# Kernel tuning notes

Measured on AMD Instinct MI355X. Metric: run time of the kernel, lower is better.

## Reference

```python
import jax, jax.numpy as jnp
import numpy as np

ALPHA = 0.25
GAMMA = 2.0

B, A, C, M = 8, 120000, 80, 24


def setup_inputs() -> dict:
    key = jax.random.key(0)
    k1, k2, k3, k4, k5, k6, k7, k8 = jax.random.split(key, 8)
    # classification probabilities in (0,1)
    classifications = jax.random.uniform(k1, (B, A, C), dtype=jnp.float32)
    regressions = jax.random.normal(k2, (B, A, 4), dtype=jnp.float32)
    # anchors: valid x1y1x2y2 boxes on an ~800px canvas
    ctr = jax.random.uniform(k3, (A, 2), minval=0.0, maxval=800.0)
    wh = jax.random.uniform(k4, (A, 2), minval=16.0, maxval=256.0)
    anchors = jnp.concatenate([ctr - 0.5 * wh, ctr + 0.5 * wh], axis=1)[None].astype(jnp.float32)
    # annotations: [B, M, 5] = (x1, y1, x2, y2, label) with -1 label padding
    xy1 = jax.random.uniform(k5, (B, M, 2), minval=0.0, maxval=600.0)
    gwh = jax.random.uniform(k6, (B, M, 2), minval=10.0, maxval=180.0)
    labels = jax.random.randint(k7, (B, M), 0, C).astype(jnp.float32)
    pad = jax.random.uniform(k8, (B, M)) < 0.25
    pad = pad.at[:, 0].set(False)  # guarantee >=1 valid GT per image
    labels = jnp.where(pad, -1.0, labels)
    annots = jnp.concatenate([xy1, xy1 + gwh, labels[..., None]], axis=2).astype(jnp.float32)
    return {"classifications": classifications, "regressions": regressions,
            "anchors": anchors, "annots": annots}


def _box_iou(a, g):
    # a: [A,4], g: [M,4] -> [A,M]
    g_area = (g[:, 2] - g[:, 0]) * (g[:, 3] - g[:, 1])
    a_area = (a[:, 2] - a[:, 0]) * (a[:, 3] - a[:, 1])
    iw = jnp.clip(jnp.minimum(a[:, None, 2], g[None, :, 2]) - jnp.maximum(a[:, None, 0], g[None, :, 0]), 0.0)
    ih = jnp.clip(jnp.minimum(a[:, None, 3], g[None, :, 3]) - jnp.maximum(a[:, None, 1], g[None, :, 1]), 0.0)
    inter = iw * ih
    union = jnp.clip(a_area[:, None] + g_area[None, :] - inter, 1e-6)
    return inter / union


def _per_image(cls_p, reg, annot, anchor, a_w, a_h, a_cx, a_cy):
    cls_p = jnp.clip(cls_p, 1e-4, 1.0 - 1e-4)
    valid = annot[:, 4] >= 0.0  # [M]
    iou = jnp.where(valid[None, :], _box_iou(anchor, annot[:, :4]), -1.0)  # [A,M]
    iou_max = iou.max(axis=1)
    iou_arg = iou.argmax(axis=1)
    pos = iou_max >= 0.5
    neg = iou_max < 0.4
    ignore = ~(pos | neg)

    assigned = annot[iou_arg]  # [A,5] gather of best GT per anchor
    labels = assigned[:, 4].astype(jnp.int32)
    onehot = jax.nn.one_hot(labels, cls_p.shape[1], dtype=cls_p.dtype)
    # -1 = ignored, 1 = positive class, 0 elsewhere
    targets = jnp.where(ignore[:, None], -1.0, onehot * pos[:, None].astype(cls_p.dtype))

    is_pos_t = targets == 1.0
    alpha_f = jnp.where(is_pos_t, ALPHA, 1.0 - ALPHA)
    focal_w = alpha_f * jnp.where(is_pos_t, 1.0 - cls_p, cls_p) ** GAMMA
    ce = -(targets * jnp.log(cls_p) + (1.0 - targets) * jnp.log(1.0 - cls_p))
    cls_loss = jnp.where(targets != -1.0, focal_w * ce, 0.0).sum()
    n_pos = pos.sum()
    cls_loss = cls_loss / jnp.maximum(n_pos.astype(cls_p.dtype), 1.0)

    gt_w = jnp.clip(assigned[:, 2] - assigned[:, 0], 1.0)
    gt_h = jnp.clip(assigned[:, 3] - assigned[:, 1], 1.0)
    gt_cx = assigned[:, 0] + 0.5 * (assigned[:, 2] - assigned[:, 0])
    gt_cy = assigned[:, 1] + 0.5 * (assigned[:, 3] - assigned[:, 1])
    t = jnp.stack([(gt_cx - a_cx) / a_w, (gt_cy - a_cy) / a_h,
                   jnp.log(gt_w / a_w), jnp.log(gt_h / a_h)], axis=1)
    t = t / jnp.array([0.1, 0.1, 0.2, 0.2], dtype=cls_p.dtype)
    diff = jnp.abs(t - reg)
    sl1 = jnp.where(diff <= 1.0 / 9.0, 0.5 * 9.0 * diff * diff, diff - 0.5 / 9.0)
    reg_sum = (sl1 * pos[:, None].astype(cls_p.dtype)).sum()
    denom = jnp.maximum(n_pos * 4, 1).astype(cls_p.dtype)  # mean over [P,4]
    reg_loss = jnp.where(n_pos > 0, reg_sum / denom, 0.0)
    return cls_loss, reg_loss


def reference(classifications, regressions, anchors, annots):
    anchor = anchors[0]
    a_w = anchor[:, 2] - anchor[:, 0]
    a_h = anchor[:, 3] - anchor[:, 1]
    a_cx = anchor[:, 0] + 0.5 * a_w
    a_cy = anchor[:, 1] + 0.5 * a_h
    cls_l, reg_l = jax.vmap(_per_image, in_axes=(0, 0, 0, None, None, None, None, None))(
        classifications, regressions, annots, anchor, a_w, a_h, a_cx, a_cy)
    return cls_l.mean(keepdims=True), reg_l.mean(keepdims=True)
```

## Files before the change

### kernel.cpp

```cpp
#include <hip/hip_runtime.h>
#include <cstdint>

#define B_ 8
#define A_ 120000
#define C_ 80
#define M_ 24
#define APB 250
#define NVB (APB * C_ / 4)


__global__ __launch_bounds__(256) void focal_main(
    const float* __restrict__ cls,
    const float* __restrict__ regs,
    const float* __restrict__ anchors,
    const float* __restrict__ annots,
    float* __restrict__ ws)
{
    const int b   = blockIdx.y;
    const int a0  = blockIdx.x * APB;
    const int tid = threadIdx.x;

    __shared__ float s_annot[M_ * 5];
    __shared__ float s_mask[APB];
    __shared__ float s_redc[4], s_redr[4], s_redp[4];

    if (tid < M_ * 5) s_annot[tid] = annots[b * M_ * 5 + tid];
    __syncthreads();

    float cls_part = 0.0f, reg_part = 0.0f, pos_part = 0.0f;
    const float PLO = 1e-4f, PHI = 1.0f - 1e-4f;

    if (tid < APB) {
        const int a = a0 + tid;
        const float4 ab = *reinterpret_cast<const float4*>(anchors + (size_t)a * 4);
        const float ax1 = ab.x, ay1 = ab.y, ax2 = ab.z, ay2 = ab.w;
        const float aw  = ax2 - ax1, ah = ay2 - ay1;
        const float acx = ax1 + 0.5f * aw, acy = ay1 + 0.5f * ah;
        const float a_area = aw * ah;

        float best = -1e30f;
        int bestm = 0;
        #pragma unroll
        for (int m = 0; m < M_; ++m) {
            const float gx1 = s_annot[m * 5 + 0], gy1 = s_annot[m * 5 + 1];
            const float gx2 = s_annot[m * 5 + 2], gy2 = s_annot[m * 5 + 3];
            const float lab = s_annot[m * 5 + 4];
            const float g_area = (gx2 - gx1) * (gy2 - gy1);
            float iw = fminf(ax2, gx2) - fmaxf(ax1, gx1); iw = fmaxf(iw, 0.0f);
            float ih = fminf(ay2, gy2) - fmaxf(ay1, gy1); ih = fmaxf(ih, 0.0f);
            const float inter = iw * ih;
            const float uni = fmaxf(a_area + g_area - inter, 1e-6f);
            float iou = inter * __builtin_amdgcn_rcpf(uni);
            iou = (lab >= 0.0f) ? iou : -1.0f;
            if (iou > best) { best = iou; bestm = m; }
        }

        const bool pos    = best >= 0.5f;
        const bool ignore = (best >= 0.4f) && !pos;
        const int  lab    = (int)s_annot[bestm * 5 + 4];
        s_mask[tid] = ignore ? 0.0f : 1.0f;

        if (pos) {
            pos_part = 1.0f;
            const float4 rv = *reinterpret_cast<const float4*>(regs + ((size_t)b * A_ + a) * 4);
            const float gx1 = s_annot[bestm * 5 + 0], gy1 = s_annot[bestm * 5 + 1];
            const float gx2 = s_annot[bestm * 5 + 2], gy2 = s_annot[bestm * 5 + 3];
            const float gw  = fmaxf(gx2 - gx1, 1.0f);
            const float gh  = fmaxf(gy2 - gy1, 1.0f);
            const float gcx = gx1 + 0.5f * (gx2 - gx1);
            const float gcy = gy1 + 0.5f * (gy2 - gy1);
            const float inv_aw = __builtin_amdgcn_rcpf(aw);
            const float inv_ah = __builtin_amdgcn_rcpf(ah);
            const float t0 = (gcx - acx) * inv_aw * 10.0f;
            const float t1 = (gcy - acy) * inv_ah * 10.0f;
            const float t2 = __logf(gw * inv_aw) * 5.0f;
            const float t3 = __logf(gh * inv_ah) * 5.0f;
            const float d0 = fabsf(t0 - rv.x), d1 = fabsf(t1 - rv.y);
            const float d2 = fabsf(t2 - rv.z), d3 = fabsf(t3 - rv.w);
            const float th = 1.0f / 9.0f, sub = 0.5f / 9.0f;
            float s;
            s  = (d0 <= th) ? 4.5f * d0 * d0 : d0 - sub;
            s += (d1 <= th) ? 4.5f * d1 * d1 : d1 - sub;
            s += (d2 <= th) ? 4.5f * d2 * d2 : d2 - sub;
            s += (d3 <= th) ? 4.5f * d3 * d3 : d3 - sub;
            reg_part = s;

            float p = cls[((size_t)b * A_ + a) * C_ + lab];
            p = fminf(fmaxf(p, PLO), PHI);
            const float q = 1.0f - p;
            const float pos_term = 0.25f * q * q * (-__logf(p));
            const float neg_term = 0.75f * p * p * (-__logf(q));
            cls_part = pos_term - neg_term;
        }
    }
    __syncthreads();

    const float4* cp4 = reinterpret_cast<const float4*>(cls + ((size_t)b * A_ + a0) * C_);
    const float NEG_SCALE = -0.75f * 0.69314718056f;
    #pragma unroll 4
    for (int i = tid; i < NVB; i += 256) {
        const float4 v = cp4[i];
        const int   al = i / 20;
        const float m  = s_mask[al];
        float c = 0.0f, p, q;
        p = fminf(fmaxf(v.x, PLO), PHI); q = 1.0f - p; c = fmaf(p * p, __log2f(q), c);
        p = fminf(fmaxf(v.y, PLO), PHI); q = 1.0f - p; c = fmaf(p * p, __log2f(q), c);
        p = fminf(fmaxf(v.z, PLO), PHI); q = 1.0f - p; c = fmaf(p * p, __log2f(q), c);
        p = fminf(fmaxf(v.w, PLO), PHI); q = 1.0f - p; c = fmaf(p * p, __log2f(q), c);
        cls_part = fmaf(m * c, NEG_SCALE, cls_part);
    }

    for (int off = 32; off > 0; off >>= 1) {
        cls_part += __shfl_down(cls_part, off, 64);
        reg_part += __shfl_down(reg_part, off, 64);
        pos_part += __shfl_down(pos_part, off, 64);
    }
    const int wid = tid >> 6;
    if ((tid & 63) == 0) { s_redc[wid] = cls_part; s_redr[wid] = reg_part; s_redp[wid] = pos_part; }
    __syncthreads();
    if (tid == 0) {
        atomicAdd(&ws[b],      s_redc[0] + s_redc[1] + s_redc[2] + s_redc[3]);
        atomicAdd(&ws[8 + b],  s_redr[0] + s_redr[1] + s_redr[2] + s_redr[3]);
        atomicAdd(&ws[16 + b], s_redp[0] + s_redp[1] + s_redp[2] + s_redp[3]);
    }
}

__global__ void focal_final(const float* __restrict__ ws, float* __restrict__ out)
{
    if (threadIdx.x == 0) {
        float cm = 0.0f, rm = 0.0f;
        for (int b = 0; b < B_; ++b) {
            const float np = ws[16 + b];
            cm += ws[b] / fmaxf(np, 1.0f);
            rm += (np > 0.0f) ? ws[8 + b] / (np * 4.0f) : 0.0f;
        }
        out[0] = cm * (1.0f / B_);
        out[1] = rm * (1.0f / B_);
    }
}

extern "C" void kernel_launch(void* const* d_in, const int* in_sizes, int n_in,
                              void* d_out, int out_size, void* d_ws, size_t ws_size,
                              hipStream_t stream)
{
    const float* cls     = (const float*)d_in[0];
    const float* regs    = (const float*)d_in[1];
    const float* anchors = (const float*)d_in[2];
    const float* annots  = (const float*)d_in[3];
    float* ws  = (float*)d_ws;
    float* out = (float*)d_out;

    hipMemsetAsync(d_ws, 0, 24 * sizeof(float), stream);

    dim3 grid(A_ / APB, B_);
    focal_main<<<grid, 256, 0, stream>>>(cls, regs, anchors, annots, ws);
    focal_final<<<1, 64, 0, stream>>>(ws, out);
}
```

Measured before the change: 449.6 us.

## Split anchor assignment and class-loss streaming into separate kernels via global mask

The fused kernel becomes two kernels. The first assigns an IoU match to each anchor and writes the ignore mask to workspace memory. The second streams the 307 MB classification tensor with full 256-thread occupancy, fixed 5-wide unrolling and no idle threads, where the old kernel had only 250 of 256 threads active in the assignment phase. The change adds a kernel launch and a global mask round trip, and it drops the lower clamp on p, relying on inputs being positive.

```diff
diff --git a/kernel.cpp b/kernel.cpp
--- a/kernel.cpp
+++ b/kernel.cpp
@@ -5,11 +5,10 @@
 #define A_ 120000
 #define C_ 80
 #define M_ 24
-#define APB 250
-#define NVB (APB * C_ / 4)
 
+#define WS_MASK_OFF 32
 
-__global__ __launch_bounds__(256) void focal_main(
+__global__ __launch_bounds__(256, 4) void assign_k(
     const float* __restrict__ cls,
     const float* __restrict__ regs,
     const float* __restrict__ anchors,
@@ -17,11 +16,10 @@
     float* __restrict__ ws)
 {
     const int b   = blockIdx.y;
-    const int a0  = blockIdx.x * APB;
     const int tid = threadIdx.x;
+    const int a   = blockIdx.x * 256 + tid;
 
     __shared__ float s_annot[M_ * 5];
-    __shared__ float s_mask[APB];
     __shared__ float s_redc[4], s_redr[4], s_redp[4];
 
     if (tid < M_ * 5) s_annot[tid] = annots[b * M_ * 5 + tid];
@@ -30,8 +28,7 @@
     float cls_part = 0.0f, reg_part = 0.0f, pos_part = 0.0f;
     const float PLO = 1e-4f, PHI = 1.0f - 1e-4f;
 
-    if (tid < APB) {
-        const int a = a0 + tid;
+    if (a < A_) {
         const float4 ab = *reinterpret_cast<const float4*>(anchors + (size_t)a * 4);
         const float ax1 = ab.x, ay1 = ab.y, ax2 = ab.z, ay2 = ab.w;
         const float aw  = ax2 - ax1, ah = ay2 - ay1;
@@ -58,7 +55,7 @@
         const bool pos    = best >= 0.5f;
         const bool ignore = (best >= 0.4f) && !pos;
         const int  lab    = (int)s_annot[bestm * 5 + 4];
-        s_mask[tid] = ignore ? 0.0f : 1.0f;
+        ws[WS_MASK_OFF + (size_t)b * A_ + a] = ignore ? 0.0f : 1.0f;
 
         if (pos) {
             pos_part = 1.0f;
@@ -88,26 +85,8 @@
             float p = cls[((size_t)b * A_ + a) * C_ + lab];
             p = fminf(fmaxf(p, PLO), PHI);
             const float q = 1.0f - p;
-            const float pos_term = 0.25f * q * q * (-__logf(p));
-            const float neg_term = 0.75f * p * p * (-__logf(q));
-            cls_part = pos_term - neg_term;
+            cls_part = 0.25f * q * q * (-__logf(p)) - 0.75f * p * p * (-__logf(q));
         }
-    }
-    __syncthreads();
-
-    const float4* cp4 = reinterpret_cast<const float4*>(cls + ((size_t)b * A_ + a0) * C_);
-    const float NEG_SCALE = -0.75f * 0.69314718056f;
-    #pragma unroll 4
-    for (int i = tid; i < NVB; i += 256) {
-        const float4 v = cp4[i];
-        const int   al = i / 20;
-        const float m  = s_mask[al];
-        float c = 0.0f, p, q;
-        p = fminf(fmaxf(v.x, PLO), PHI); q = 1.0f - p; c = fmaf(p * p, __log2f(q), c);
-        p = fminf(fmaxf(v.y, PLO), PHI); q = 1.0f - p; c = fmaf(p * p, __log2f(q), c);
-        p = fminf(fmaxf(v.z, PLO), PHI); q = 1.0f - p; c = fmaf(p * p, __log2f(q), c);
-        p = fminf(fmaxf(v.w, PLO), PHI); q = 1.0f - p; c = fmaf(p * p, __log2f(q), c);
-        cls_part = fmaf(m * c, NEG_SCALE, cls_part);
     }
 
     for (int off = 32; off > 0; off >>= 1) {
@@ -122,6 +101,44 @@
         atomicAdd(&ws[b],      s_redc[0] + s_redc[1] + s_redc[2] + s_redc[3]);
         atomicAdd(&ws[8 + b],  s_redr[0] + s_redr[1] + s_redr[2] + s_redr[3]);
         atomicAdd(&ws[16 + b], s_redp[0] + s_redp[1] + s_redp[2] + s_redp[3]);
+    }
+}
+
+#define SB 1875
+__global__ __launch_bounds__(256, 8) void stream_k(
+    const float* __restrict__ cls,
+    float* __restrict__ ws)
+{
+    const int b   = blockIdx.y;
+    const int tid = threadIdx.x;
+    const float4* cp4 = reinterpret_cast<const float4*>(cls + (size_t)b * A_ * C_);
+    const float*  msk = ws + WS_MASK_OFF + (size_t)b * A_;
+    const int base = blockIdx.x * (5 * 256);
+
+    __shared__ float s_red[4];
+    const float PHI = 1.0f - 1e-4f;
+    float acc = 0.0f;
+
+    #pragma unroll
+    for (int k = 0; k < 5; ++k) {
+        const int i = base + k * 256 + tid;
+        const float4 v = cp4[i];
+        const float  m = msk[i / 20];
+        float c = 0.0f, p, q;
+        p = fminf(v.x, PHI); q = 1.0f - p; c = fmaf(p * p, __log2f(q), c);
+        p = fminf(v.y, PHI); q = 1.0f - p; c = fmaf(p * p, __log2f(q), c);
+        p = fminf(v.z, PHI); q = 1.0f - p; c = fmaf(p * p, __log2f(q), c);
+        p = fminf(v.w, PHI); q = 1.0f - p; c = fmaf(p * p, __log2f(q), c);
+        acc = fmaf(m, c, acc);
+    }
+
+    for (int off = 32; off > 0; off >>= 1) acc += __shfl_down(acc, off, 64);
+    const int wid = tid >> 6;
+    if ((tid & 63) == 0) s_red[wid] = acc;
+    __syncthreads();
+    if (tid == 0) {
+        const float NEG_SCALE = -0.75f * 0.69314718056f;
+        atomicAdd(&ws[b], (s_red[0] + s_red[1] + s_red[2] + s_red[3]) * NEG_SCALE);
     }
 }
 
@@ -152,7 +169,11 @@
 
     hipMemsetAsync(d_ws, 0, 24 * sizeof(float), stream);
 
-    dim3 grid(A_ / APB, B_);
-    focal_main<<<grid, 256, 0, stream>>>(cls, regs, anchors, annots, ws);
+    dim3 agrid((A_ + 255) / 256, B_);
+    assign_k<<<agrid, 256, 0, stream>>>(cls, regs, anchors, annots, ws);
+
+    dim3 sgrid(SB, B_);
+    stream_k<<<sgrid, 256, 0, stream>>>(cls, ws);
+
     focal_final<<<1, 64, 0, stream>>>(ws, out);
 }
```

After: 615.0 us. 36.8% more time.
